# Performance work log

Hardware: AMD Instinct MI355X
Metric: run time of the kernel (lower is better)

The kernel has to match this reference:

```python
import jax, jax.numpy as jnp
import numpy as np

B, NNODE, FIN, FOUT = 64, 512, 64, 64

def setup_inputs() -> dict:
    key = jax.random.key(0)
    ks = jax.random.split(key, 8)
    stdW = 1.0 / np.sqrt(FIN)
    stdA = 1.0 / np.sqrt(FOUT)
    return {
        "X": jax.random.normal(ks[0], (B, NNODE, FIN), dtype=jnp.float32),
        "A": jax.random.uniform(ks[1], (B, NNODE, NNODE), dtype=jnp.float32),
        "N": jax.random.randint(ks[2], (B,), 1, NNODE + 1, dtype=jnp.int64),
        "W": jax.random.uniform(ks[3], (FIN, FOUT), jnp.float32, -stdW, stdW),
        "a": jax.random.uniform(ks[4], (FOUT, FOUT), jnp.float32, -stdA, stdA),
        "bias_W": jax.random.uniform(ks[5], (FOUT,), jnp.float32, -stdW, stdW),
        "bias_a": jax.random.uniform(ks[6], (NNODE,), jnp.float32, -1.0 / np.sqrt(NNODE), 1.0 / np.sqrt(NNODE)),
    }

def reference(X, A, N, W, a, bias_W, bias_a):
    # A_ = A + identity on the top-left n_atoms block (only diagonal entries)
    idx = jnp.arange(A.shape[1])
    diag_mask = (idx[None, :] < N[:, None]).astype(A.dtype)  # [B, n]
    A_ = A + jnp.einsum('bn,nm->bnm', diag_mask, jnp.eye(A.shape[1], dtype=A.dtype))
    # XW: [B, n, F_out]
    XW = jnp.einsum('bnc,cd->bnd', X, W)
    # buf[a,j,k] = sum_i a[i,j] * XW^T[a,j,k]  (einsum 'ij,ajk->ajk')
    col_sum = a.sum(axis=0)  # [F_out]
    XWT = jnp.swapaxes(XW, 1, 2)  # [B, F_out, n]
    buf = col_sum[None, :, None] * XWT
    Z = jnp.einsum('bif,bfk->bik', XW, buf) + bias_a  # [B, n, n] + [n] broadcast on last dim
    att = jnp.tanh(jnp.einsum('bij,bjk->bik', A_, Z))
    H = jnp.einsum('bij,bjd->bid', att, XW) + bias_W
    return H
```

## Files before the change

kernel.cpp:

```cpp
#include <hip/hip_runtime.h>

#define BB 64
#define NN 512
#define FD 64

typedef short bf16x8 __attribute__((ext_vector_type(8)));
typedef float f32x4 __attribute__((ext_vector_type(4)));

__device__ __forceinline__ unsigned short f2bf(float f){
    unsigned u = __builtin_bit_cast(unsigned, f);
    u += 0x7fffu + ((u >> 16) & 1u);
    return (unsigned short)(u >> 16);
}
__device__ __forceinline__ float bf2f(unsigned short h){
    unsigned u = ((unsigned)h) << 16;
    return __builtin_bit_cast(float, u);
}
__device__ __forceinline__ float fast_tanh(float x){
    float e = __expf(2.0f * x);
    return 1.0f - 2.0f * __builtin_amdgcn_rcpf(e + 1.0f);
}

__global__ __launch_bounds__(256) void k_xw(const float* __restrict__ X,
                                            const float* __restrict__ W,
                                            unsigned short* __restrict__ XWh,
                                            unsigned short* __restrict__ XWt){
    __shared__ unsigned short Xl[64][72];
    __shared__ unsigned short Wtl[64][72];
    __shared__ unsigned short Cl[64][72];
    __shared__ unsigned short ClT[64][72];
    int t = threadIdx.x;
    int row0 = blockIdx.x * 64;
    int r = t >> 2, c0 = (t & 3) * 16;
    {
        const float4* wsrc = (const float4*)&W[r*64 + c0];
        #pragma unroll
        for (int q = 0; q < 4; q++){
            float4 v = wsrc[q];
            Wtl[c0 + q*4 + 0][r] = f2bf(v.x);
            Wtl[c0 + q*4 + 1][r] = f2bf(v.y);
            Wtl[c0 + q*4 + 2][r] = f2bf(v.z);
            Wtl[c0 + q*4 + 3][r] = f2bf(v.w);
        }
        const float4* src = (const float4*)&X[(row0 + r)*FD + c0];
        #pragma unroll
        for (int q = 0; q < 4; q++){
            float4 v = src[q];
            ushort4 h; h.x=f2bf(v.x); h.y=f2bf(v.y); h.z=f2bf(v.z); h.w=f2bf(v.w);
            *(ushort4*)&Xl[r][c0 + q*4] = h;
        }
    }
    __syncthreads();
    int lane = t & 63, w = t >> 6, l15 = lane & 15, quad = lane >> 4;
    f32x4 acc[4] = {{0,0,0,0},{0,0,0,0},{0,0,0,0},{0,0,0,0}};
    #pragma unroll
    for (int ks = 0; ks < 2; ks++){
        bf16x8 af = *(const bf16x8*)&Xl[w*16 + l15][ks*32 + quad*8];
        #pragma unroll
        for (int nt = 0; nt < 4; nt++){
            bf16x8 bfr = *(const bf16x8*)&Wtl[nt*16 + l15][ks*32 + quad*8];
            acc[nt] = __builtin_amdgcn_mfma_f32_16x16x32_bf16(af, bfr, acc[nt], 0, 0, 0);
        }
    }
    #pragma unroll
    for (int nt = 0; nt < 4; nt++)
        #pragma unroll
        for (int rg = 0; rg < 4; rg++){
            unsigned short hb = f2bf(acc[nt][rg]);
            Cl [w*16 + quad*4 + rg][nt*16 + l15] = hb;
            ClT[nt*16 + l15][w*16 + quad*4 + rg] = hb;
        }
    __syncthreads();
    int b = blockIdx.x >> 3, n0 = (blockIdx.x & 7) * 64;
    {
        uint4 v0 = *(const uint4*)&Cl[r][c0];
        uint4 v1 = *(const uint4*)&Cl[r][c0 + 8];
        *(uint4*)&XWh[(row0 + r)*FD + c0]     = v0;
        *(uint4*)&XWh[(row0 + r)*FD + c0 + 8] = v1;
    }
    {
        uint4 v0 = *(const uint4*)&ClT[r][c0];
        uint4 v1 = *(const uint4*)&ClT[r][c0 + 8];
        *(uint4*)&XWt[(b*64 + r)*NN + n0 + c0]     = v0;
        *(uint4*)&XWt[(b*64 + r)*NN + n0 + c0 + 8] = v1;
    }
}

__global__ __launch_bounds__(512, 8) void k_fused(const float* __restrict__ A,
                                                  const unsigned short* __restrict__ XWh,
                                                  const unsigned short* __restrict__ XWt,
                                                  const float* __restrict__ a,
                                                  const int* __restrict__ Ni,
                                                  const float* __restrict__ bias_a,
                                                  const float* __restrict__ bias_W,
                                                  float* __restrict__ H){
    __shared__ unsigned short s0[64][72];
    __shared__ unsigned short s1[64][72];
    __shared__ unsigned short MPl[32][72];
    __shared__ float cspart[8][64];
    __shared__ float csl[64];
    __shared__ float rspart[32][16];
    __shared__ float rsl[32];
    __shared__ float bl[512];
    int t = threadIdx.x;
    int b = blockIdx.y, it = blockIdx.x;
    int i0 = it * 32;
    int Nb = (Ni[1] == 0) ? Ni[2*b] : Ni[b];
    int lane = t & 63, w = t >> 6, l15 = lane & 15, quad = lane >> 4;
    int wr = w & 1, wc = w >> 1;
    int r16 = t >> 4, cA = (t & 15) * 4;
    int r8 = t >> 3, c8 = (t & 7) * 8;
    const float* Ab = A + (b*NN + i0)*NN;
    const unsigned short* XWtb = XWt + b*64*NN;
    const unsigned short* XWhb = XWh + b*NN*FD;

    {
        int cd = t & 63, cp = t >> 6;
        float s = 0.f;
        #pragma unroll
        for (int i = 0; i < 8; i++) s += a[(cp*8 + i)*64 + cd];
        cspart[cp][cd] = s;
    }
    bl[t] = bias_a[t];

    float4 pA = *(const float4*)&Ab[r16*NN + cA];
    uint4  pB = *(const uint4*)&XWtb[r8*NN + c8];
    f32x4 acc = {0,0,0,0};
    float rs = 0.f;
    int diagc = it >> 1;
    for (int c = 0; c < 8; c++){
        __syncthreads();
        {
            float4 v = pA;
            rs += v.x + v.y + v.z + v.w;
            ushort4 h; h.x=f2bf(v.x); h.y=f2bf(v.y); h.z=f2bf(v.z); h.w=f2bf(v.w);
            *(ushort4*)&s0[r16][cA] = h;
        }
        *(uint4*)&s1[r8][c8] = pB;
        __syncthreads();
        if (c < 7){
            pA = *(const float4*)&Ab[r16*NN + (c+1)*64 + cA];
            pB = *(const uint4*)&XWtb[r8*NN + (c+1)*64 + c8];
        }
        #pragma unroll
        for (int ks = 0; ks < 2; ks++){
            bf16x8 af  = *(const bf16x8*)&s0[wr*16 + l15][ks*32 + quad*8];
            bf16x8 bfr = *(const bf16x8*)&s1[wc*16 + l15][ks*32 + quad*8];
            acc = __builtin_amdgcn_mfma_f32_16x16x32_bf16(af, bfr, acc, 0, 0, 0);
        }
        if (c == diagc){
            #pragma unroll
            for (int rg = 0; rg < 4; rg++){
                int li = wr*16 + quad*4 + rg;
                if (i0 + li < Nb)
                    acc[rg] += bf2f(s1[wc*16 + l15][(it & 1)*32 + li]);
            }
        }
    }
    rspart[r16][t & 15] = rs;
    __syncthreads();
    if (t < 64){
        float s = 0.f;
        #pragma unroll
        for (int p = 0; p < 8; p++) s += cspart[p][t];
        csl[t] = s;
    } else if (t < 96){
        int row = t - 64;
        float s = 0.f;
        #pragma unroll
        for (int p = 0; p < 16; p++) s += rspart[row][p];
        if (i0 + row < Nb) s += 1.f;
        rsl[row] = s;
    }
    __syncthreads();
    {
        float cs = csl[wc*16 + l15];
        #pragma unroll
        for (int rg = 0; rg < 4; rg++)
            MPl[wr*16 + quad*4 + rg][wc*16 + l15] = f2bf(acc[rg] * cs);
    }
    __syncthreads();
    bf16x8 maf[2];
    maf[0] = *(const bf16x8*)&MPl[wr*16 + l15][quad*8];
    maf[1] = *(const bf16x8*)&MPl[wr*16 + l15][32 + quad*8];
    float rs_r[4];
    #pragma unroll
    for (int rg = 0; rg < 4; rg++) rs_r[rg] = rsl[wr*16 + quad*4 + rg];

    uint4 q1 = *(const uint4*)&XWhb[r8*FD + c8];
    uint4 q2 = *(const uint4*)&XWtb[r8*NN + c8];
    f32x4 hacc = {0,0,0,0};
    for (int jt = 0; jt < 8; jt++){
        __syncthreads();
        *(uint4*)&s0[r8][c8] = q1;
        *(uint4*)&s1[r8][c8] = q2;
        __syncthreads();
        if (jt < 7){
            q1 = *(const uint4*)&XWhb[((jt+1)*64 + r8)*FD + c8];
            q2 = *(const uint4*)&XWtb[r8*NN + (jt+1)*64 + c8];
        }
        {
            float bv = bl[jt*64 + wc*16 + l15];
            f32x4 arg = { rs_r[0]*bv, rs_r[1]*bv, rs_r[2]*bv, rs_r[3]*bv };
            #pragma unroll
            for (int ks = 0; ks < 2; ks++){
                bf16x8 bfr = *(const bf16x8*)&s0[wc*16 + l15][ks*32 + quad*8];
                arg = __builtin_amdgcn_mfma_f32_16x16x32_bf16(maf[ks], bfr, arg, 0, 0, 0);
            }
            #pragma unroll
            for (int rg = 0; rg < 4; rg++)
                MPl[wr*16 + quad*4 + rg][wc*16 + l15] = f2bf(fast_tanh(arg[rg]));
        }
        __syncthreads();
        #pragma unroll
        for (int ks = 0; ks < 2; ks++){
            bf16x8 paf = *(const bf16x8*)&MPl[wr*16 + l15][ks*32 + quad*8];
            bf16x8 bfr = *(const bf16x8*)&s1[wc*16 + l15][ks*32 + quad*8];
            hacc = __builtin_amdgcn_mfma_f32_16x16x32_bf16(paf, bfr, hacc, 0, 0, 0);
        }
    }
    {
        float bw = bias_W[wc*16 + l15];
        #pragma unroll
        for (int rg = 0; rg < 4; rg++)
            H[(b*NN + i0 + wr*16 + quad*4 + rg)*FD + wc*16 + l15] = hacc[rg] + bw;
    }
}

extern "C" void kernel_launch(void* const* d_in, const int* in_sizes, int n_in,
                              void* d_out, int out_size, void* d_ws, size_t ws_size,
                              hipStream_t stream){
    const float* X      = (const float*)d_in[0];
    const float* A      = (const float*)d_in[1];
    const int*   N      = (const int*)  d_in[2];
    const float* W      = (const float*)d_in[3];
    const float* a      = (const float*)d_in[4];
    const float* bias_W = (const float*)d_in[5];
    const float* bias_a = (const float*)d_in[6];
    float* H = (float*)d_out;
    char* ws = (char*)d_ws;

    unsigned short* XWh = (unsigned short*)(ws);
    unsigned short* XWt = (unsigned short*)(ws + (4u<<20));

    k_xw   <<<BB * NN / 64, 256, 0, stream>>>(X, W, XWh, XWt);
    k_fused<<<dim3(16, BB), 512, 0, stream>>>(A, XWh, XWt, a, N, bias_a, bias_W, H);
}
```

Baseline: 138.0 us.

## Double row tile to 64, double-buffer LDS stages, reorder grid batch-major

Each block now handles 64 rows of A instead of 32, with each wave computing two 16x16 output tiles. This halves the redundant loads and the recompute of the XW/Z tiles per batch. The A and XWt tiles are double-buffered in a shared 4-slot LDS buffer, removing one barrier per iteration, and A loads are prefetched two stages ahead. The grid is swapped so batch varies fastest, and launch bounds drop to 6 blocks per CU. In exchange there are fewer blocks (512 instead of 1024), more registers per thread and more LDS per block.

```diff
diff --git a/kernel.cpp b/kernel.cpp
--- a/kernel.cpp
+++ b/kernel.cpp
@@ -86,7 +86,7 @@
     }
 }
 
-__global__ __launch_bounds__(512, 8) void k_fused(const float* __restrict__ A,
+__global__ __launch_bounds__(512, 6) void k_fused(const float* __restrict__ A,
                                                   const unsigned short* __restrict__ XWh,
                                                   const unsigned short* __restrict__ XWt,
                                                   const float* __restrict__ a,
@@ -94,22 +94,19 @@
                                                   const float* __restrict__ bias_a,
                                                   const float* __restrict__ bias_W,
                                                   float* __restrict__ H){
-    __shared__ unsigned short s0[64][72];
-    __shared__ unsigned short s1[64][72];
-    __shared__ unsigned short MPl[32][72];
+    __shared__ unsigned short buf[4][64][72];
     __shared__ float cspart[8][64];
     __shared__ float csl[64];
-    __shared__ float rspart[32][16];
-    __shared__ float rsl[32];
+    __shared__ float rspart[64][8];
+    __shared__ float rsl[64];
     __shared__ float bl[512];
     int t = threadIdx.x;
-    int b = blockIdx.y, it = blockIdx.x;
-    int i0 = it * 32;
+    int b = blockIdx.x, it = blockIdx.y;
+    int i0 = it * 64;
     int Nb = (Ni[1] == 0) ? Ni[2*b] : Ni[b];
     int lane = t & 63, w = t >> 6, l15 = lane & 15, quad = lane >> 4;
-    int wr = w & 1, wc = w >> 1;
-    int r16 = t >> 4, cA = (t & 15) * 4;
-    int r8 = t >> 3, c8 = (t & 7) * 8;
+    int wr = w & 3, wc = w >> 2;
+    int r8 = t >> 3, c4 = (t & 7) * 4, c8 = (t & 7) * 8;
     const float* Ab = A + (b*NN + i0)*NN;
     const unsigned short* XWtb = XWt + b*64*NN;
     const unsigned short* XWhb = XWh + b*NN*FD;
@@ -123,107 +120,137 @@
     }
     bl[t] = bias_a[t];
 
-    float4 pA = *(const float4*)&Ab[r16*NN + cA];
-    uint4  pB = *(const uint4*)&XWtb[r8*NN + c8];
-    f32x4 acc = {0,0,0,0};
+    float4 pA[2][2]; uint4 pB;
+    pA[0][0] = *(const float4*)&Ab[r8*NN + c4];
+    pA[0][1] = *(const float4*)&Ab[r8*NN + 32 + c4];
+    pA[1][0] = *(const float4*)&Ab[r8*NN + 64 + c4];
+    pA[1][1] = *(const float4*)&Ab[r8*NN + 64 + 32 + c4];
+    pB = *(const uint4*)&XWtb[r8*NN + c8];
+    f32x4 acc[2] = {{0,0,0,0},{0,0,0,0}};
     float rs = 0.f;
-    int diagc = it >> 1;
+    #pragma unroll
     for (int c = 0; c < 8; c++){
+        {
+            float4 v = pA[c & 1][0];
+            rs += v.x + v.y + v.z + v.w;
+            ushort4 h; h.x=f2bf(v.x); h.y=f2bf(v.y); h.z=f2bf(v.z); h.w=f2bf(v.w);
+            *(ushort4*)&buf[c & 1][r8][c4] = h;
+            v = pA[c & 1][1];
+            rs += v.x + v.y + v.z + v.w;
+            ushort4 h2; h2.x=f2bf(v.x); h2.y=f2bf(v.y); h2.z=f2bf(v.z); h2.w=f2bf(v.w);
+            *(ushort4*)&buf[c & 1][r8][32 + c4] = h2;
+        }
+        *(uint4*)&buf[2 + (c & 1)][r8][c8] = pB;
+        if (c < 7) pB = *(const uint4*)&XWtb[r8*NN + (c+1)*64 + c8];
+        __syncthreads();
+        if (c < 6){
+            pA[c & 1][0] = *(const float4*)&Ab[r8*NN + (c+2)*64 + c4];
+            pA[c & 1][1] = *(const float4*)&Ab[r8*NN + (c+2)*64 + 32 + c4];
+        }
+        #pragma unroll
+        for (int ks = 0; ks < 2; ks++){
+            bf16x8 af = *(const bf16x8*)&buf[c & 1][wr*16 + l15][ks*32 + quad*8];
+            #pragma unroll
+            for (int nt = 0; nt < 2; nt++){
+                bf16x8 bfr = *(const bf16x8*)&buf[2 + (c & 1)][wc*32 + nt*16 + l15][ks*32 + quad*8];
+                acc[nt] = __builtin_amdgcn_mfma_f32_16x16x32_bf16(af, bfr, acc[nt], 0, 0, 0);
+            }
+        }
+        if (c == it){
+            #pragma unroll
+            for (int nt = 0; nt < 2; nt++)
+                #pragma unroll
+                for (int rg = 0; rg < 4; rg++){
+                    int iloc = wr*16 + quad*4 + rg;
+                    if (i0 + iloc < Nb)
+                        acc[nt][rg] += bf2f(buf[2 + (c & 1)][wc*32 + nt*16 + l15][iloc]);
+                }
+        }
+    }
+    rspart[r8][t & 7] = rs;
+    __syncthreads();
+    if (t < 64){
+        float s = 0.f;
+        #pragma unroll
+        for (int p = 0; p < 8; p++) s += cspart[p][t];
+        csl[t] = s;
+    } else if (t < 128){
+        int row = t - 64;
+        float s = 0.f;
+        #pragma unroll
+        for (int p = 0; p < 8; p++) s += rspart[row][p];
+        if (i0 + row < Nb) s += 1.f;
+        rsl[row] = s;
+    }
+    __syncthreads();
+    #pragma unroll
+    for (int nt = 0; nt < 2; nt++){
+        float cs = csl[wc*32 + nt*16 + l15];
+        #pragma unroll
+        for (int rg = 0; rg < 4; rg++)
+            buf[2][wr*16 + quad*4 + rg][wc*32 + nt*16 + l15] = f2bf(acc[nt][rg] * cs);
+    }
+    __syncthreads();
+    bf16x8 maf[2];
+    maf[0] = *(const bf16x8*)&buf[2][wr*16 + l15][quad*8];
+    maf[1] = *(const bf16x8*)&buf[2][wr*16 + l15][32 + quad*8];
+    float rs_r[4];
+    #pragma unroll
+    for (int rg = 0; rg < 4; rg++) rs_r[rg] = rsl[wr*16 + quad*4 + rg];
+
+    {
+        uint4 q1 = *(const uint4*)&XWhb[r8*FD + c8];
+        uint4 q2 = *(const uint4*)&XWtb[r8*NN + c8];
+        *(uint4*)&buf[0][r8][c8] = q1;
+        *(uint4*)&buf[1][r8][c8] = q2;
+    }
+    uint4 q1 = *(const uint4*)&XWhb[(64 + r8)*FD + c8];
+    uint4 q2 = *(const uint4*)&XWtb[r8*NN + 64 + c8];
+    f32x4 hacc[2] = {{0,0,0,0},{0,0,0,0}};
+    #pragma unroll
+    for (int jt = 0; jt < 8; jt++){
+        __syncthreads();
+        #pragma unroll
+        for (int nt = 0; nt < 2; nt++){
+            float bv = bl[jt*64 + wc*32 + nt*16 + l15];
+            f32x4 arg = { rs_r[0]*bv, rs_r[1]*bv, rs_r[2]*bv, rs_r[3]*bv };
+            #pragma unroll
+            for (int ks = 0; ks < 2; ks++){
+                bf16x8 bfr = *(const bf16x8*)&buf[0][wc*32 + nt*16 + l15][ks*32 + quad*8];
+                arg = __builtin_amdgcn_mfma_f32_16x16x32_bf16(maf[ks], bfr, arg, 0, 0, 0);
+            }
+            #pragma unroll
+            for (int rg = 0; rg < 4; rg++)
+                buf[2][wr*16 + quad*4 + rg][wc*32 + nt*16 + l15] = f2bf(fast_tanh(arg[rg]));
+        }
         __syncthreads();
         {
-            float4 v = pA;
-            rs += v.x + v.y + v.z + v.w;
-            ushort4 h; h.x=f2bf(v.x); h.y=f2bf(v.y); h.z=f2bf(v.z); h.w=f2bf(v.w);
-            *(ushort4*)&s0[r16][cA] = h;
-        }
-        *(uint4*)&s1[r8][c8] = pB;
-        __syncthreads();
-        if (c < 7){
-            pA = *(const float4*)&Ab[r16*NN + (c+1)*64 + cA];
-            pB = *(const uint4*)&XWtb[r8*NN + (c+1)*64 + c8];
-        }
-        #pragma unroll
-        for (int ks = 0; ks < 2; ks++){
-            bf16x8 af  = *(const bf16x8*)&s0[wr*16 + l15][ks*32 + quad*8];
-            bf16x8 bfr = *(const bf16x8*)&s1[wc*16 + l15][ks*32 + quad*8];
-            acc = __builtin_amdgcn_mfma_f32_16x16x32_bf16(af, bfr, acc, 0, 0, 0);
-        }
-        if (c == diagc){
-            #pragma unroll
-            for (int rg = 0; rg < 4; rg++){
-                int li = wr*16 + quad*4 + rg;
-                if (i0 + li < Nb)
-                    acc[rg] += bf2f(s1[wc*16 + l15][(it & 1)*32 + li]);
-            }
-        }
-    }
-    rspart[r16][t & 15] = rs;
-    __syncthreads();
-    if (t < 64){
-        float s = 0.f;
-        #pragma unroll
-        for (int p = 0; p < 8; p++) s += cspart[p][t];
-        csl[t] = s;
-    } else if (t < 96){
-        int row = t - 64;
-        float s = 0.f;
-        #pragma unroll
-        for (int p = 0; p < 16; p++) s += rspart[row][p];
-        if (i0 + row < Nb) s += 1.f;
-        rsl[row] = s;
-    }
-    __syncthreads();
-    {
-        float cs = csl[wc*16 + l15];
+            const unsigned short (*bT)[72] = buf[(jt & 1) ? 3 : 1];
+            #pragma unroll
+            for (int ks = 0; ks < 2; ks++){
+                bf16x8 paf = *(const bf16x8*)&buf[2][wr*16 + l15][ks*32 + quad*8];
+                #pragma unroll
+                for (int dt = 0; dt < 2; dt++){
+                    bf16x8 bfr = *(const bf16x8*)&bT[wc*32 + dt*16 + l15][ks*32 + quad*8];
+                    hacc[dt] = __builtin_amdgcn_mfma_f32_16x16x32_bf16(paf, bfr, hacc[dt], 0, 0, 0);
+                }
+            }
+        }
+        if (jt < 7){
+            *(uint4*)&buf[0][r8][c8] = q1;
+            *(uint4*)&buf[(jt & 1) ? 1 : 3][r8][c8] = q2;
+            if (jt < 6){
+                q1 = *(const uint4*)&XWhb[((jt+2)*64 + r8)*FD + c8];
+                q2 = *(const uint4*)&XWtb[r8*NN + (jt+2)*64 + c8];
+            }
+        }
+    }
+    #pragma unroll
+    for (int dt = 0; dt < 2; dt++){
+        float bw = bias_W[wc*32 + dt*16 + l15];
         #pragma unroll
         for (int rg = 0; rg < 4; rg++)
-            MPl[wr*16 + quad*4 + rg][wc*16 + l15] = f2bf(acc[rg] * cs);
-    }
-    __syncthreads();
-    bf16x8 maf[2];
-    maf[0] = *(const bf16x8*)&MPl[wr*16 + l15][quad*8];
-    maf[1] = *(const bf16x8*)&MPl[wr*16 + l15][32 + quad*8];
-    float rs_r[4];
-    #pragma unroll
-    for (int rg = 0; rg < 4; rg++) rs_r[rg] = rsl[wr*16 + quad*4 + rg];
-
-    uint4 q1 = *(const uint4*)&XWhb[r8*FD + c8];
-    uint4 q2 = *(const uint4*)&XWtb[r8*NN + c8];
-    f32x4 hacc = {0,0,0,0};
-    for (int jt = 0; jt < 8; jt++){
-        __syncthreads();
-        *(uint4*)&s0[r8][c8] = q1;
-        *(uint4*)&s1[r8][c8] = q2;
-        __syncthreads();
-        if (jt < 7){
-            q1 = *(const uint4*)&XWhb[((jt+1)*64 + r8)*FD + c8];
-            q2 = *(const uint4*)&XWtb[r8*NN + (jt+1)*64 + c8];
-        }
-        {
-            float bv = bl[jt*64 + wc*16 + l15];
-            f32x4 arg = { rs_r[0]*bv, rs_r[1]*bv, rs_r[2]*bv, rs_r[3]*bv };
-            #pragma unroll
-            for (int ks = 0; ks < 2; ks++){
-                bf16x8 bfr = *(const bf16x8*)&s0[wc*16 + l15][ks*32 + quad*8];
-                arg = __builtin_amdgcn_mfma_f32_16x16x32_bf16(maf[ks], bfr, arg, 0, 0, 0);
-            }
-            #pragma unroll
-            for (int rg = 0; rg < 4; rg++)
-                MPl[wr*16 + quad*4 + rg][wc*16 + l15] = f2bf(fast_tanh(arg[rg]));
-        }
-        __syncthreads();
-        #pragma unroll
-        for (int ks = 0; ks < 2; ks++){
-            bf16x8 paf = *(const bf16x8*)&MPl[wr*16 + l15][ks*32 + quad*8];
-            bf16x8 bfr = *(const bf16x8*)&s1[wc*16 + l15][ks*32 + quad*8];
-            hacc = __builtin_amdgcn_mfma_f32_16x16x32_bf16(paf, bfr, hacc, 0, 0, 0);
-        }
-    }
-    {
-        float bw = bias_W[wc*16 + l15];
-        #pragma unroll
-        for (int rg = 0; rg < 4; rg++)
-            H[(b*NN + i0 + wr*16 + quad*4 + rg)*FD + wc*16 + l15] = hacc[rg] + bw;
+            H[(b*NN + i0 + wr*16 + quad*4 + rg)*FD + wc*32 + dt*16 + l15] = hacc[dt][rg] + bw;
     }
 }
 
@@ -244,5 +271,5 @@
     unsigned short* XWt = (unsigned short*)(ws + (4u<<20));
 
     k_xw   <<<BB * NN / 64, 256, 0, stream>>>(X, W, XWh, XWt);
-    k_fused<<<dim3(16, BB), 512, 0, stream>>>(A, XWh, XWt, a, N, bias_a, bias_W, H);
-}
+    k_fused<<<dim3(BB, 8), 512, 0, stream>>>(A, XWh, XWt, a, N, bias_a, bias_W, H);
+}
```

New measurement: 138.5 us. No clear change (+0.4%).
